# Optimization experiments

Measured on AMD Instinct MI355X. Metric: run time of the kernel, lower is better.

Reference implementation:

```python
import jax, jax.numpy as jnp
import numpy as np

HID = 64   # RNN_HID_SIZE
FEAT = 9   # feature dim, hard-coded in module
T = 36     # SEQ_LEN


def setup_inputs() -> dict:
    key = jax.random.key(0)
    ks = jax.random.split(key, 20)
    B = 16384

    def u(k, shape, stdv):
        return jax.random.uniform(k, shape, jnp.float32, -stdv, stdv)

    s_h = 1.0 / np.sqrt(HID)    # stdv for layers with 64 rows / fan-in 64
    s_f = 1.0 / np.sqrt(FEAT)   # stdv 1/3 for feature-sized layers
    s_c = 1.0 / np.sqrt(2 * FEAT)  # weight_combine: Linear(18, 9)

    inp = {
        "values": jax.random.normal(ks[0], (B, T, FEAT), jnp.float32),
        "masks": (jax.random.uniform(ks[1], (B, T, FEAT)) < 0.8).astype(jnp.float32),
        "deltas": jax.random.uniform(ks[2], (B, T, FEAT), jnp.float32, 0.0, 5.0),
        # TemporalDecay h: W [64, 9], stdv = 1/sqrt(64)
        "W_gh": u(ks[3], (HID, FEAT), s_h), "b_gh": u(ks[4], (HID,), s_h),
        # TemporalDecay x (diag): W [9, 9], stdv = 1/sqrt(9)
        "W_gx": u(ks[5], (FEAT, FEAT), s_f), "b_gx": u(ks[6], (FEAT,), s_f),
        # hist_reg: Linear(64, 9)
        "W_hist": u(ks[7], (FEAT, HID), s_h), "b_hist": u(ks[8], (FEAT,), s_h),
        "W_feat": u(ks[9], (FEAT, FEAT), s_f), "b_feat": u(ks[10], (FEAT,), s_f),
        # weight_combine: Linear(18, 9)
        "W_comb": u(ks[11], (FEAT, 2 * FEAT), s_c), "b_comb": u(ks[12], (FEAT,), s_c),
        # LSTMCell(18, 64): gates order i, f, g, o
        "W_ih": u(ks[13], (4 * HID, 2 * FEAT), s_h), "W_hh": u(ks[14], (4 * HID, HID), s_h),
        "b_ih": u(ks[15], (4 * HID,), s_h), "b_hh": u(ks[16], (4 * HID,), s_h),
    }
    return inp


def reference(values, masks, deltas, W_gh, b_gh, W_gx, b_gx, W_hist, b_hist,
              W_feat, b_feat, W_comb, b_comb, W_ih, W_hh, b_ih, b_hh):
    B = values.shape[0]
    dt = values.dtype
    eye = jnp.eye(FEAT, dtype=dt)
    Wgx_diag = W_gx * eye            # TemporalDecay diag mask
    Wfeat_off = W_feat * (1.0 - eye)

    # time-major for scan: [T, B, F]
    xs = (jnp.swapaxes(values, 0, 1), jnp.swapaxes(masks, 0, 1), jnp.swapaxes(deltas, 0, 1))

    def step(carry, xt):
        h, c, loss = carry
        x, m, d = xt
        gamma_h = jnp.exp(-jax.nn.relu(d @ W_gh.T + b_gh))   # [B, 64]
        gamma_x = jnp.exp(-jax.nn.relu(d @ Wgx_diag.T + b_gx))  # [B, 9]
        h = h * gamma_h
        x_h = h @ W_hist.T + b_hist
        denom = jnp.sum(m) + 1e-5
        x_c = m * x + (1.0 - m) * x_h
        z_h = x_c @ Wfeat_off.T + b_feat
        alpha = jnp.concatenate([gamma_x, m], axis=1) @ W_comb.T + b_comb
        c_h = alpha * z_h + (1.0 - alpha) * x_h
        loss = loss + (jnp.sum(jnp.abs(x - x_h) * m)
                       + jnp.sum(jnp.abs(x - z_h) * m)
                       + jnp.sum(jnp.abs(x - c_h) * m)) / denom
        c_c = m * x + (1.0 - m) * c_h
        inp = jnp.concatenate([c_c, m], axis=1)              # [B, 18]
        gates = inp @ W_ih.T + b_ih + h @ W_hh.T + b_hh      # [B, 256]
        i, f, g, o = jnp.split(gates, 4, axis=1)
        c = jax.nn.sigmoid(f) * c + jax.nn.sigmoid(i) * jnp.tanh(g)
        h = jax.nn.sigmoid(o) * jnp.tanh(c)
        return (h, c, loss), c_c

    init = (jnp.zeros((B, HID), dt), jnp.zeros((B, HID), dt), jnp.zeros((), dt))
    (_, _, loss), imps = jax.lax.scan(step, init, xs)
    imputations = jnp.swapaxes(imps, 0, 1)  # [B, T, F]
    return loss / T, imputations
```

## Files before the change

kernel.cpp:

```cpp
#include <hip/hip_runtime.h>

typedef _Float16 hh;
typedef _Float16 h2  __attribute__((ext_vector_type(2)));
typedef _Float16 v4h __attribute__((ext_vector_type(4)));
typedef _Float16 v8h __attribute__((ext_vector_type(8)));
typedef float v4f    __attribute__((ext_vector_type(4)));
typedef unsigned short u16;

#define T_STEPS 36
#define FEAT 9
#define HID 64
#define BT 32
#define SIN_STR 232
#define PK_STR 40

__device__ __forceinline__ float fast_exp2(float x) {
#if __has_builtin(__builtin_amdgcn_exp2f)
  return __builtin_amdgcn_exp2f(x);
#else
  return exp2f(x);
#endif
}
__device__ __forceinline__ float fast_rcp(float x) {
#if __has_builtin(__builtin_amdgcn_rcpf)
  return __builtin_amdgcn_rcpf(x);
#else
  return 1.f / x;
#endif
}
__device__ __forceinline__ float sigmoid_fast(float x) {
  return fast_rcp(1.f + fast_exp2(x * -1.442695041f));
}
__device__ __forceinline__ float tanh_fast(float x) {
  return 1.f - 2.f * fast_rcp(1.f + fast_exp2(x * 2.885390082f));
}
__device__ __forceinline__ float fdot2(h2 a, h2 b, float c) {
#if __has_builtin(__builtin_amdgcn_fdot2)
  return __builtin_amdgcn_fdot2(a, b, c, false);
#else
  return c + (float)a[0] * (float)b[0] + (float)a[1] * (float)b[1];
#endif
}
__device__ __forceinline__ h2 mkh2(hh a, hh b) { h2 r; r[0] = a; r[1] = b; return r; }
__device__ __forceinline__ v4f mfma16(v8h a, v8h b, v4f c) {
  return __builtin_amdgcn_mfma_f32_16x16x32_f16(a, b, c, 0, 0, 0);
}

__global__ void zero_ws(float* __restrict__ ws, float* __restrict__ out) {
  int tid = threadIdx.x;
  if (tid < T_STEPS) ws[tid] = 0.f;
  if (tid == 0) out[0] = 0.f;
}

__global__ __launch_bounds__(256) void denom_kernel(const float* __restrict__ masks,
                                                    float* __restrict__ ws) {
  __shared__ float red[T_STEPS];
  const int tid = threadIdx.x;
  const int e = blockIdx.x * 256 + tid;
  if (tid < T_STEPS) red[tid] = 0.f;
  float acc[T_STEPS];
#pragma unroll
  for (int t = 0; t < T_STEPS; ++t) acc[t] = 0.f;
  const float4* p = (const float4*)masks + (size_t)e * 81;
#pragma unroll
  for (int c = 0; c < 81; ++c) {
    float4 v = p[c];
    acc[(4 * c) / 9]     += v.x;
    acc[(4 * c + 1) / 9] += v.y;
    acc[(4 * c + 2) / 9] += v.z;
    acc[(4 * c + 3) / 9] += v.w;
  }
  __syncthreads();
  int rot = tid % T_STEPS;
#pragma unroll
  for (int t = 0; t < T_STEPS; ++t) {
    int tt = rot + t; if (tt >= T_STEPS) tt -= T_STEPS;
    atomicAdd(&red[tt], acc[tt]);
  }
  __syncthreads();
  if (tid < T_STEPS) atomicAdd(&ws[tid], red[tid]);
}


__global__ __launch_bounds__(256, 2) void rits_kernel(
    const float* __restrict__ values, const float* __restrict__ masks,
    const float* __restrict__ deltas,
    const float* __restrict__ W_gh, const float* __restrict__ b_gh,
    const float* __restrict__ W_gx, const float* __restrict__ b_gx,
    const float* __restrict__ W_hist, const float* __restrict__ b_hist,
    const float* __restrict__ W_feat, const float* __restrict__ b_feat,
    const float* __restrict__ W_comb, const float* __restrict__ b_comb,
    const float* __restrict__ W_ih, const float* __restrict__ W_hh,
    const float* __restrict__ b_ih, const float* __restrict__ b_hh,
    const float* __restrict__ denom, float* __restrict__ out) {

  __shared__ __align__(16) hh sIn[BT * SIN_STR];
  __shared__ __align__(16) hh sPk[BT * PK_STR];
  __shared__ float sRed[256];

  const int tid = threadIdx.x;
  const int lane = tid & 63;
  const int wid = tid >> 6;
  const int q = lane >> 4;
  const int nlo = lane & 15;
  const int b0 = blockIdx.x * BT;
  const int j_col = 16 * wid + nlo;

  v8h bG[4][3];
#pragma unroll
  for (int p = 0; p < 4; ++p)
#pragma unroll
    for (int kt = 0; kt < 3; ++kt) {
      int n = 64 * p + j_col;
      v8h r;
#pragma unroll
      for (int jj = 0; jj < 8; ++jj) {
        int k = kt * 32 + q * 8 + jj;
        float v = 0.f;
        if (k < 18)       v = W_ih[n * 18 + k];
        else if (k < 82)  v = W_hh[n * 64 + (k - 18)];
        else if (k == 82) v = b_ih[n] + b_hh[n];
        r[jj] = (hh)v;
      }
      bG[p][kt] = r;
    }
  v8h bH[3];
#pragma unroll
  for (int kt = 0; kt < 3; ++kt) {
    v8h r;
#pragma unroll
    for (int jj = 0; jj < 8; ++jj) {
      int k = kt * 32 + q * 8 + jj;
      float v = 0.f;
      if (nlo < 9) {
        if (k >= 18 && k < 82) v = W_hist[nlo * 64 + (k - 18)];
        else if (k == 82)      v = b_hist[nlo];
      }
      r[jj] = (hh)v;
    }
    bH[kt] = r;
  }
  v8h bGamA, bGamB;
  {
    int n = j_col;
    v8h ra, rb;
#pragma unroll
    for (int jj = 0; jj < 8; ++jj) {
      int k = q * 8 + jj;
      float va = 0.f, vb = 0.f;
      if (k == 2) va = b_gh[n];
      else if (k >= 16 && k < 25) va = W_gh[n * 9 + (k - 16)];
      if (k >= 2 && k < 11) vb = W_gh[n * 9 + (k - 2)];
      else if (k == 12) vb = b_gh[n];
      ra[jj] = (hh)va; rb[jj] = (hh)vb;
    }
    bGamA = ra; bGamB = rb;
  }

  const int eP = tid >> 3, fqw = tid & 7;
  h2 wf1[5], wf2[5], wc1[9], wc2[9];
  float bf1 = b_feat[fqw], bf2 = b_feat[8];
  float bc1v = b_comb[fqw], bc2v = b_comb[8];
#pragma unroll
  for (int j = 0; j < 5; ++j) {
    int i0 = 2 * j, i1 = 2 * j + 1;
    hh a0 = (hh)((i0 == fqw) ? 0.f : W_feat[fqw * 9 + i0]);
    hh a1 = (hh)((i1 < 9) ? ((i1 == fqw) ? 0.f : W_feat[fqw * 9 + i1]) : 0.f);
    wf1[j] = mkh2(a0, a1);
    hh c0 = (hh)((i0 == 8) ? 0.f : W_feat[8 * 9 + i0]);
    hh c1 = (hh)((i1 < 9) ? W_feat[8 * 9 + i1] : 0.f);
    wf2[j] = mkh2(c0, c1);
  }
#pragma unroll
  for (int j = 0; j < 9; ++j) {
    wc1[j] = mkh2((hh)W_comb[fqw * 18 + 2 * j], (hh)W_comb[fqw * 18 + 2 * j + 1]);
    wc2[j] = mkh2((hh)W_comb[8 * 18 + 2 * j], (hh)W_comb[8 * 18 + 2 * j + 1]);
  }
  float wgx[9], bgxv[9];
#pragma unroll
  for (int f = 0; f < 9; ++f) { wgx[f] = W_gx[f * 9 + f]; bgxv[f] = b_gx[f]; }

  for (int i = tid; i < BT * SIN_STR; i += 256) sIn[i] = (hh)0.f;
  __syncthreads();
  if (tid < BT) {
    sIn[tid * SIN_STR + 82] = (hh)1.f;
    sIn[tid * SIN_STR + 178] = (hh)1.f;
    sIn[tid * SIN_STR + 212] = (hh)1.f;
  }
  const int e1 = tid / 9, f1 = tid - 9 * e1;
  const int e2g = (tid + 256) / 9, f2g = (tid + 256) - 9 * e2g;
  float dreg0 = 0.f, dreg1 = 0.f;
  {
    size_t off = (size_t)(b0 + e1) * (T_STEPS * FEAT) + f1;
    sPk[e1 * PK_STR + f1] = (hh)values[off];
    sPk[e1 * PK_STR + 9 + f1] = (hh)masks[off];
    sPk[e1 * PK_STR + 27 + f1] = (hh)deltas[off];
    float d1 = deltas[off + FEAT];
    dreg0 = d1;
    sIn[e1 * SIN_STR + 202 + f1] = (hh)d1;
    if (tid < 32) {
      size_t off2 = (size_t)(b0 + e2g) * (T_STEPS * FEAT) + f2g;
      sPk[e2g * PK_STR + f2g] = (hh)values[off2];
      sPk[e2g * PK_STR + 9 + f2g] = (hh)masks[off2];
      sPk[e2g * PK_STR + 27 + f2g] = (hh)deltas[off2];
      float d1b = deltas[off2 + FEAT];
      dreg1 = d1b;
      sIn[e2g * SIN_STR + 202 + f2g] = (hh)d1b;
    }
  }
  __syncthreads();

  float c_s[8];
#pragma unroll
  for (int i = 0; i < 8; ++i) c_s[i] = 0.f;
  float loss_acc = 0.f;

  for (int t = 0; t < T_STEPS; ++t) {
    const float inv_den = fast_rcp(denom[t] + 1e-5f);

    v4f gacc[2];
    {
      const int sel = (t + 1) & 1;
      const int awin = 176 + sel * 24;
#pragma unroll
      for (int mt = 0; mt < 2; ++mt) {
        v8h a = *(const v8h*)&sIn[(mt * 16 + nlo) * SIN_STR + awin + q * 8];
        v4f z4 = {0.f, 0.f, 0.f, 0.f};
        gacc[mt] = sel ? mfma16(a, bGamB, z4) : mfma16(a, bGamA, z4);
      }
    }
    if (wid < 2) {
      const int base = (t & 1) * 96;
      v4f acc = {0.f, 0.f, 0.f, 0.f};
#pragma unroll
      for (int kt = 0; kt < 3; ++kt) {
        v8h a = *(const v8h*)&sIn[(wid * 16 + nlo) * SIN_STR + base + kt * 32 + q * 8];
        acc = mfma16(a, bH[kt], acc);
      }
      if (nlo < 9) {
#pragma unroll
        for (int r = 0; r < 4; ++r)
          sPk[(wid * 16 + q * 4 + r) * PK_STR + 18 + nlo] = (hh)acc[r];
      }
    }
    __syncthreads();

    {
      const int pk = eP * PK_STR;
      float x_f  = (float)sPk[pk + fqw];
      float m_f  = (float)sPk[pk + 9 + fqw];
      float xh_f = (float)sPk[pk + 18 + fqw];
      v8h r0 = *(const v8h*)&sPk[pk];
      v8h r1 = *(const v8h*)&sPk[pk + 8];
      v8h r2 = *(const v8h*)&sPk[pk + 16];
      v8h r3 = *(const v8h*)&sPk[pk + 24];
      v4h r4 = *(const v4h*)&sPk[pk + 32];
      hh xxh[9] = {r0[0],r0[1],r0[2],r0[3],r0[4],r0[5],r0[6],r0[7],r1[0]};
      hh mmh[9] = {r1[1],r1[2],r1[3],r1[4],r1[5],r1[6],r1[7],r2[0],r2[1]};
      hh xhh[9] = {r2[2],r2[3],r2[4],r2[5],r2[6],r2[7],r3[0],r3[1],r3[2]};
      hh ddh[9] = {r3[3],r3[4],r3[5],r3[6],r3[7],r4[0],r4[1],r4[2],r4[3]};
      hh xch[10];
#pragma unroll
      for (int f = 0; f < 9; ++f) {
        u16 mb = __builtin_bit_cast(u16, mmh[f]);
        xch[f] = mb ? xxh[f] : xhh[f];
      }
      xch[9] = (hh)0.f;
      hh gxh[9];
#pragma unroll
      for (int f = 0; f < 9; ++f) {
        float y = fmaxf((float)ddh[f] * wgx[f] + bgxv[f], 0.f);
        gxh[f] = (hh)fast_exp2(y * -1.442695041f);
      }
      h2 xc2[5] = {mkh2(xch[0],xch[1]), mkh2(xch[2],xch[3]), mkh2(xch[4],xch[5]),
                   mkh2(xch[6],xch[7]), mkh2(xch[8],xch[9])};
      h2 g2[9]  = {mkh2(gxh[0],gxh[1]), mkh2(gxh[2],gxh[3]), mkh2(gxh[4],gxh[5]),
                   mkh2(gxh[6],gxh[7]), mkh2(gxh[8],mmh[0]), mkh2(mmh[1],mmh[2]),
                   mkh2(mmh[3],mmh[4]), mkh2(mmh[5],mmh[6]), mkh2(mmh[7],mmh[8])};
      float z1 = bf1, a1 = bc1v;
#pragma unroll
      for (int j = 0; j < 5; ++j) z1 = fdot2(wf1[j], xc2[j], z1);
#pragma unroll
      for (int j = 0; j < 9; ++j) a1 = fdot2(wc1[j], g2[j], a1);
      float ch1 = xh_f + a1 * (z1 - xh_f);
      bool obs1 = (m_f != 0.f);
      float cc1 = obs1 ? x_f : ch1;
      float lterm = obs1 ? (fabsf(x_f - xh_f) + fabsf(x_f - z1) + fabsf(x_f - ch1)) : 0.f;
      const int pb = (t & 1) * 96;
      sIn[eP * SIN_STR + pb + fqw] = (hh)cc1;
      sIn[eP * SIN_STR + pb + 9 + fqw] = (hh)m_f;
      out[1 + (size_t)(b0 + eP) * (T_STEPS * FEAT) + t * FEAT + fqw] = cc1;
      if (fqw == 7) {
        float z2 = bf2, a2 = bc2v;
#pragma unroll
        for (int j = 0; j < 5; ++j) z2 = fdot2(wf2[j], xc2[j], z2);
#pragma unroll
        for (int j = 0; j < 9; ++j) a2 = fdot2(wc2[j], g2[j], a2);
        float x8 = (float)xxh[8], m8 = (float)mmh[8], xh8 = (float)xhh[8];
        float ch2 = xh8 + a2 * (z2 - xh8);
        bool obs2 = (m8 != 0.f);
        float cc2 = obs2 ? x8 : ch2;
        lterm += obs2 ? (fabsf(x8 - xh8) + fabsf(x8 - z2) + fabsf(x8 - ch2)) : 0.f;
        sIn[eP * SIN_STR + pb + 8] = (hh)cc2;
        sIn[eP * SIN_STR + pb + 17] = mmh[8];
        out[1 + (size_t)(b0 + eP) * (T_STEPS * FEAT) + t * FEAT + 8] = cc2;
      }
      loss_acc += lterm * inv_den;
    }
    __syncthreads();

    {
      float px0 = 0.f, pm0 = 0.f, px1 = 0.f, pm1 = 0.f, pd0 = 0.f, pd1 = 0.f;
      const bool pre1 = (t + 1 < T_STEPS), pre2 = (t + 2 < T_STEPS);
      if (pre1) {
        size_t off = (size_t)(b0 + e1) * (T_STEPS * FEAT) + (t + 1) * FEAT + f1;
        px0 = values[off]; pm0 = masks[off];
        if (tid < 32) {
          size_t off2 = (size_t)(b0 + e2g) * (T_STEPS * FEAT) + (t + 1) * FEAT + f2g;
          px1 = values[off2]; pm1 = masks[off2];
        }
      }
      if (pre2) {
        size_t offd = (size_t)(b0 + e1) * (T_STEPS * FEAT) + (t + 2) * FEAT + f1;
        pd0 = deltas[offd];
        if (tid < 32) {
          size_t offd2 = (size_t)(b0 + e2g) * (T_STEPS * FEAT) + (t + 2) * FEAT + f2g;
          pd1 = deltas[offd2];
        }
      }

      const int base = (t & 1) * 96;
      const int pub = ((t + 1) & 1) * 96;
      v8h af[2][3];
#pragma unroll
      for (int mt = 0; mt < 2; ++mt)
#pragma unroll
        for (int kt = 0; kt < 3; ++kt)
          af[mt][kt] = *(const v8h*)&sIn[(mt * 16 + nlo) * SIN_STR + base + kt * 32 + q * 8];

      v4f acc[2][4];
#pragma unroll
      for (int mt = 0; mt < 2; ++mt)
#pragma unroll
        for (int p = 0; p < 4; ++p)
          acc[mt][p] = (v4f){0.f, 0.f, 0.f, 0.f};
#pragma unroll
      for (int mt = 0; mt < 2; ++mt)
#pragma unroll
        for (int p = 0; p < 4; ++p)
#pragma unroll
          for (int kt = 0; kt < 3; ++kt)
            acc[mt][p] = mfma16(af[mt][kt], bG[p][kt], acc[mt][p]);

#pragma unroll
      for (int mt = 0; mt < 2; ++mt) {
#pragma unroll
        for (int r = 0; r < 4; ++r) {
          float ig = sigmoid_fast(acc[mt][0][r]);
          float fg = sigmoid_fast(acc[mt][1][r]);
          float gg = tanh_fast(acc[mt][2][r]);
          float og = sigmoid_fast(acc[mt][3][r]);
          float cn = fg * c_s[mt * 4 + r] + ig * gg;
          c_s[mt * 4 + r] = cn;
          float hn = og * tanh_fast(cn);
          float gam = fast_exp2(fmaxf(gacc[mt][r], 0.f) * -1.442695041f);
          sIn[(mt * 16 + q * 4 + r) * SIN_STR + pub + 18 + j_col] = (hh)(hn * gam);
        }
      }

      if (pre1) {
        sPk[e1 * PK_STR + f1] = (hh)px0;
        sPk[e1 * PK_STR + 9 + f1] = (hh)pm0;
        sPk[e1 * PK_STR + 27 + f1] = (hh)dreg0;
        if (tid < 32) {
          sPk[e2g * PK_STR + f2g] = (hh)px1;
          sPk[e2g * PK_STR + 9 + f2g] = (hh)pm1;
          sPk[e2g * PK_STR + 27 + f2g] = (hh)dreg1;
        }
      }
      if (pre2) {
        const int sb = 192 + (t & 1) * 10;
        sIn[e1 * SIN_STR + sb + f1] = (hh)pd0;
        dreg0 = pd0;
        if (tid < 32) { sIn[e2g * SIN_STR + sb + f2g] = (hh)pd1; dreg1 = pd1; }
      }
    }
    __syncthreads();
  }

  sRed[tid] = loss_acc;
  __syncthreads();
  for (int k = 128; k > 0; k >>= 1) {
    if (tid < k) sRed[tid] += sRed[tid + k];
    __syncthreads();
  }
  if (tid == 0) atomicAdd(out, sRed[0] * (1.f / (float)T_STEPS));
}

extern "C" void kernel_launch(void* const* d_in, const int* in_sizes, int n_in,
                              void* d_out, int out_size, void* d_ws, size_t ws_size,
                              hipStream_t stream) {
  const float* values = (const float*)d_in[0];
  const float* masks  = (const float*)d_in[1];
  const float* deltas = (const float*)d_in[2];
  const float* W_gh   = (const float*)d_in[3];
  const float* b_gh   = (const float*)d_in[4];
  const float* W_gx   = (const float*)d_in[5];
  const float* b_gx   = (const float*)d_in[6];
  const float* W_hist = (const float*)d_in[7];
  const float* b_hist = (const float*)d_in[8];
  const float* W_feat = (const float*)d_in[9];
  const float* b_feat = (const float*)d_in[10];
  const float* W_comb = (const float*)d_in[11];
  const float* b_comb = (const float*)d_in[12];
  const float* W_ih   = (const float*)d_in[13];
  const float* W_hh   = (const float*)d_in[14];
  const float* b_ih   = (const float*)d_in[15];
  const float* b_hh   = (const float*)d_in[16];

  float* out = (float*)d_out;
  float* ws  = (float*)d_ws;
  int B = in_sizes[0] / (T_STEPS * FEAT);

  zero_ws<<<1, 64, 0, stream>>>(ws, out);
  denom_kernel<<<B / 256, 256, 0, stream>>>(masks, ws);
  rits_kernel<<<B / BT, 256, 0, stream>>>(values, masks, deltas,
                                          W_gh, b_gh, W_gx, b_gx,
                                          W_hist, b_hist, W_feat, b_feat,
                                          W_comb, b_comb, W_ih, W_hh,
                                          b_ih, b_hh, ws, out);
}
```

Baseline: 292.6 us.

## Halve batch tile per block, raise occupancy, use wave shuffles for reductions

Each block of the RITS kernel now handles 16 batch rows instead of 32, so it has twice as many blocks, and the launch bound requests 4 blocks per CU. Each wave does one MFMA row tile, and the elementwise imputation stage alternates between the two wave pairs on odd and even steps. The denom kernel and the final loss reduction use wavefront shuffles in place of shared-memory atomics and tree reductions. The aim is to hide the latency of the serial 36-step recurrence through more resident blocks. The cost is half the threads sitting idle in the elementwise phase and fewer MFMAs per barrier.

```diff
diff --git a/kernel.cpp b/kernel.cpp
--- a/kernel.cpp
+++ b/kernel.cpp
@@ -10,7 +10,7 @@
 #define T_STEPS 36
 #define FEAT 9
 #define HID 64
-#define BT 32
+#define BT 16
 #define SIN_STR 232
 #define PK_STR 40
 
@@ -52,16 +52,14 @@
   if (tid == 0) out[0] = 0.f;
 }
 
-__global__ __launch_bounds__(256) void denom_kernel(const float* __restrict__ masks,
-                                                    float* __restrict__ ws) {
-  __shared__ float red[T_STEPS];
+__global__ __launch_bounds__(64) void denom_kernel(const float* __restrict__ masks,
+                                                   float* __restrict__ ws) {
   const int tid = threadIdx.x;
-  const int e = blockIdx.x * 256 + tid;
-  if (tid < T_STEPS) red[tid] = 0.f;
+  const size_t e = (size_t)blockIdx.x * 64 + tid;
+  const float4* p = (const float4*)masks + e * 81;
   float acc[T_STEPS];
 #pragma unroll
   for (int t = 0; t < T_STEPS; ++t) acc[t] = 0.f;
-  const float4* p = (const float4*)masks + (size_t)e * 81;
 #pragma unroll
   for (int c = 0; c < 81; ++c) {
     float4 v = p[c];
@@ -70,19 +68,16 @@
     acc[(4 * c + 2) / 9] += v.z;
     acc[(4 * c + 3) / 9] += v.w;
   }
-  __syncthreads();
-  int rot = tid % T_STEPS;
 #pragma unroll
   for (int t = 0; t < T_STEPS; ++t) {
-    int tt = rot + t; if (tt >= T_STEPS) tt -= T_STEPS;
-    atomicAdd(&red[tt], acc[tt]);
-  }
-  __syncthreads();
-  if (tid < T_STEPS) atomicAdd(&ws[tid], red[tid]);
-}
-
-
-__global__ __launch_bounds__(256, 2) void rits_kernel(
+    float v = acc[t];
+#pragma unroll
+    for (int s = 32; s > 0; s >>= 1) v += __shfl_down(v, s, 64);
+    if (tid == 0) atomicAdd(&ws[t], v);
+  }
+}
+
+__global__ __launch_bounds__(256, 4) void rits_kernel(
     const float* __restrict__ values, const float* __restrict__ masks,
     const float* __restrict__ deltas,
     const float* __restrict__ W_gh, const float* __restrict__ b_gh,
@@ -96,7 +91,7 @@
 
   __shared__ __align__(16) hh sIn[BT * SIN_STR];
   __shared__ __align__(16) hh sPk[BT * PK_STR];
-  __shared__ float sRed[256];
+  __shared__ float sRedW[4];
 
   const int tid = threadIdx.x;
   const int lane = tid & 63;
@@ -157,7 +152,9 @@
     bGamA = ra; bGamB = rb;
   }
 
-  const int eP = tid >> 3, fqw = tid & 7;
+  const int uP = tid & 127;
+  const int eP = uP >> 3, fqw = uP & 7;
+  const int myPair = wid >> 1;
   h2 wf1[5], wf2[5], wc1[9], wc2[9];
   float bf1 = b_feat[fqw], bf2 = b_feat[8];
   float bc1v = b_comb[fqw], bc2v = b_comb[8];
@@ -180,6 +177,9 @@
 #pragma unroll
   for (int f = 0; f < 9; ++f) { wgx[f] = W_gx[f * 9 + f]; bgxv[f] = b_gx[f]; }
 
+  float* const outp0 = out + 1 + (size_t)(b0 + eP) * (T_STEPS * FEAT) + fqw;
+  float* const outp8 = out + 1 + (size_t)(b0 + eP) * (T_STEPS * FEAT) + 8;
+
   for (int i = tid; i < BT * SIN_STR; i += 256) sIn[i] = (hh)0.f;
   __syncthreads();
   if (tid < BT) {
@@ -188,64 +188,52 @@
     sIn[tid * SIN_STR + 212] = (hh)1.f;
   }
   const int e1 = tid / 9, f1 = tid - 9 * e1;
-  const int e2g = (tid + 256) / 9, f2g = (tid + 256) - 9 * e2g;
-  float dreg0 = 0.f, dreg1 = 0.f;
-  {
+  const bool pf = (tid < BT * FEAT);
+  float dreg = 0.f;
+  if (pf) {
     size_t off = (size_t)(b0 + e1) * (T_STEPS * FEAT) + f1;
     sPk[e1 * PK_STR + f1] = (hh)values[off];
     sPk[e1 * PK_STR + 9 + f1] = (hh)masks[off];
     sPk[e1 * PK_STR + 27 + f1] = (hh)deltas[off];
     float d1 = deltas[off + FEAT];
-    dreg0 = d1;
+    dreg = d1;
     sIn[e1 * SIN_STR + 202 + f1] = (hh)d1;
-    if (tid < 32) {
-      size_t off2 = (size_t)(b0 + e2g) * (T_STEPS * FEAT) + f2g;
-      sPk[e2g * PK_STR + f2g] = (hh)values[off2];
-      sPk[e2g * PK_STR + 9 + f2g] = (hh)masks[off2];
-      sPk[e2g * PK_STR + 27 + f2g] = (hh)deltas[off2];
-      float d1b = deltas[off2 + FEAT];
-      dreg1 = d1b;
-      sIn[e2g * SIN_STR + 202 + f2g] = (hh)d1b;
-    }
   }
   __syncthreads();
 
-  float c_s[8];
-#pragma unroll
-  for (int i = 0; i < 8; ++i) c_s[i] = 0.f;
+  float c_s[4];
+#pragma unroll
+  for (int i = 0; i < 4; ++i) c_s[i] = 0.f;
   float loss_acc = 0.f;
 
   for (int t = 0; t < T_STEPS; ++t) {
     const float inv_den = fast_rcp(denom[t] + 1e-5f);
 
-    v4f gacc[2];
+    v4f gacc;
     {
       const int sel = (t + 1) & 1;
       const int awin = 176 + sel * 24;
-#pragma unroll
-      for (int mt = 0; mt < 2; ++mt) {
-        v8h a = *(const v8h*)&sIn[(mt * 16 + nlo) * SIN_STR + awin + q * 8];
-        v4f z4 = {0.f, 0.f, 0.f, 0.f};
-        gacc[mt] = sel ? mfma16(a, bGamB, z4) : mfma16(a, bGamA, z4);
-      }
-    }
-    if (wid < 2) {
+      v8h a = *(const v8h*)&sIn[nlo * SIN_STR + awin + q * 8];
+      v4f z4 = {0.f, 0.f, 0.f, 0.f};
+      gacc = sel ? mfma16(a, bGamB, z4) : mfma16(a, bGamA, z4);
+    }
+    if (wid == 0) {
       const int base = (t & 1) * 96;
       v4f acc = {0.f, 0.f, 0.f, 0.f};
 #pragma unroll
       for (int kt = 0; kt < 3; ++kt) {
-        v8h a = *(const v8h*)&sIn[(wid * 16 + nlo) * SIN_STR + base + kt * 32 + q * 8];
+        v8h a = *(const v8h*)&sIn[nlo * SIN_STR + base + kt * 32 + q * 8];
         acc = mfma16(a, bH[kt], acc);
       }
       if (nlo < 9) {
 #pragma unroll
         for (int r = 0; r < 4; ++r)
-          sPk[(wid * 16 + q * 4 + r) * PK_STR + 18 + nlo] = (hh)acc[r];
+          sPk[(q * 4 + r) * PK_STR + 18 + nlo] = (hh)acc[r];
       }
     }
     __syncthreads();
 
-    {
+    if (myPair == (t & 1)) {
       const int pk = eP * PK_STR;
       float x_f  = (float)sPk[pk + fqw];
       float m_f  = (float)sPk[pk + 9 + fqw];
@@ -289,7 +277,7 @@
       const int pb = (t & 1) * 96;
       sIn[eP * SIN_STR + pb + fqw] = (hh)cc1;
       sIn[eP * SIN_STR + pb + 9 + fqw] = (hh)m_f;
-      out[1 + (size_t)(b0 + eP) * (T_STEPS * FEAT) + t * FEAT + fqw] = cc1;
+      outp0[t * FEAT] = cc1;
       if (fqw == 7) {
         float z2 = bf2, a2 = bc2v;
 #pragma unroll
@@ -303,98 +291,77 @@
         lterm += obs2 ? (fabsf(x8 - xh8) + fabsf(x8 - z2) + fabsf(x8 - ch2)) : 0.f;
         sIn[eP * SIN_STR + pb + 8] = (hh)cc2;
         sIn[eP * SIN_STR + pb + 17] = mmh[8];
-        out[1 + (size_t)(b0 + eP) * (T_STEPS * FEAT) + t * FEAT + 8] = cc2;
+        outp8[t * FEAT] = cc2;
       }
       loss_acc += lterm * inv_den;
     }
     __syncthreads();
 
     {
-      float px0 = 0.f, pm0 = 0.f, px1 = 0.f, pm1 = 0.f, pd0 = 0.f, pd1 = 0.f;
-      const bool pre1 = (t + 1 < T_STEPS), pre2 = (t + 2 < T_STEPS);
+      float px = 0.f, pm = 0.f, pd = 0.f;
+      const bool pre1 = pf && (t + 1 < T_STEPS);
+      const bool pre2 = pf && (t + 2 < T_STEPS);
       if (pre1) {
         size_t off = (size_t)(b0 + e1) * (T_STEPS * FEAT) + (t + 1) * FEAT + f1;
-        px0 = values[off]; pm0 = masks[off];
-        if (tid < 32) {
-          size_t off2 = (size_t)(b0 + e2g) * (T_STEPS * FEAT) + (t + 1) * FEAT + f2g;
-          px1 = values[off2]; pm1 = masks[off2];
-        }
+        px = values[off]; pm = masks[off];
       }
       if (pre2) {
         size_t offd = (size_t)(b0 + e1) * (T_STEPS * FEAT) + (t + 2) * FEAT + f1;
-        pd0 = deltas[offd];
-        if (tid < 32) {
-          size_t offd2 = (size_t)(b0 + e2g) * (T_STEPS * FEAT) + (t + 2) * FEAT + f2g;
-          pd1 = deltas[offd2];
-        }
+        pd = deltas[offd];
       }
 
       const int base = (t & 1) * 96;
       const int pub = ((t + 1) & 1) * 96;
-      v8h af[2][3];
-#pragma unroll
-      for (int mt = 0; mt < 2; ++mt)
+      v8h af[3];
+#pragma unroll
+      for (int kt = 0; kt < 3; ++kt)
+        af[kt] = *(const v8h*)&sIn[nlo * SIN_STR + base + kt * 32 + q * 8];
+
+      v4f acc[4];
+#pragma unroll
+      for (int p = 0; p < 4; ++p) acc[p] = (v4f){0.f, 0.f, 0.f, 0.f};
+#pragma unroll
+      for (int p = 0; p < 4; ++p)
 #pragma unroll
         for (int kt = 0; kt < 3; ++kt)
-          af[mt][kt] = *(const v8h*)&sIn[(mt * 16 + nlo) * SIN_STR + base + kt * 32 + q * 8];
-
-      v4f acc[2][4];
-#pragma unroll
-      for (int mt = 0; mt < 2; ++mt)
-#pragma unroll
-        for (int p = 0; p < 4; ++p)
-          acc[mt][p] = (v4f){0.f, 0.f, 0.f, 0.f};
-#pragma unroll
-      for (int mt = 0; mt < 2; ++mt)
-#pragma unroll
-        for (int p = 0; p < 4; ++p)
-#pragma unroll
-          for (int kt = 0; kt < 3; ++kt)
-            acc[mt][p] = mfma16(af[mt][kt], bG[p][kt], acc[mt][p]);
-
-#pragma unroll
-      for (int mt = 0; mt < 2; ++mt) {
-#pragma unroll
-        for (int r = 0; r < 4; ++r) {
-          float ig = sigmoid_fast(acc[mt][0][r]);
-          float fg = sigmoid_fast(acc[mt][1][r]);
-          float gg = tanh_fast(acc[mt][2][r]);
-          float og = sigmoid_fast(acc[mt][3][r]);
-          float cn = fg * c_s[mt * 4 + r] + ig * gg;
-          c_s[mt * 4 + r] = cn;
-          float hn = og * tanh_fast(cn);
-          float gam = fast_exp2(fmaxf(gacc[mt][r], 0.f) * -1.442695041f);
-          sIn[(mt * 16 + q * 4 + r) * SIN_STR + pub + 18 + j_col] = (hh)(hn * gam);
-        }
+          acc[p] = mfma16(af[kt], bG[p][kt], acc[p]);
+
+#pragma unroll
+      for (int r = 0; r < 4; ++r) {
+        float ig = sigmoid_fast(acc[0][r]);
+        float fg = sigmoid_fast(acc[1][r]);
+        float gg = tanh_fast(acc[2][r]);
+        float og = sigmoid_fast(acc[3][r]);
+        float cn = fg * c_s[r] + ig * gg;
+        c_s[r] = cn;
+        float hn = og * tanh_fast(cn);
+        float gam = fast_exp2(fmaxf(gacc[r], 0.f) * -1.442695041f);
+        sIn[(q * 4 + r) * SIN_STR + pub + 18 + j_col] = (hh)(hn * gam);
       }
 
       if (pre1) {
-        sPk[e1 * PK_STR + f1] = (hh)px0;
-        sPk[e1 * PK_STR + 9 + f1] = (hh)pm0;
-        sPk[e1 * PK_STR + 27 + f1] = (hh)dreg0;
-        if (tid < 32) {
-          sPk[e2g * PK_STR + f2g] = (hh)px1;
-          sPk[e2g * PK_STR + 9 + f2g] = (hh)pm1;
-          sPk[e2g * PK_STR + 27 + f2g] = (hh)dreg1;
-        }
+        sPk[e1 * PK_STR + f1] = (hh)px;
+        sPk[e1 * PK_STR + 9 + f1] = (hh)pm;
+        sPk[e1 * PK_STR + 27 + f1] = (hh)dreg;
       }
       if (pre2) {
         const int sb = 192 + (t & 1) * 10;
-        sIn[e1 * SIN_STR + sb + f1] = (hh)pd0;
-        dreg0 = pd0;
-        if (tid < 32) { sIn[e2g * SIN_STR + sb + f2g] = (hh)pd1; dreg1 = pd1; }
+        sIn[e1 * SIN_STR + sb + f1] = (hh)pd;
+        dreg = pd;
       }
     }
     __syncthreads();
   }
 
-  sRed[tid] = loss_acc;
-  __syncthreads();
-  for (int k = 128; k > 0; k >>= 1) {
-    if (tid < k) sRed[tid] += sRed[tid + k];
+  {
+    float v = loss_acc;
+#pragma unroll
+    for (int s = 32; s > 0; s >>= 1) v += __shfl_down(v, s, 64);
+    if (lane == 0) sRedW[wid] = v;
     __syncthreads();
-  }
-  if (tid == 0) atomicAdd(out, sRed[0] * (1.f / (float)T_STEPS));
+    if (tid == 0)
+      atomicAdd(out, (sRedW[0] + sRedW[1] + sRedW[2] + sRedW[3]) * (1.f / (float)T_STEPS));
+  }
 }
 
 extern "C" void kernel_launch(void* const* d_in, const int* in_sizes, int n_in,
@@ -423,7 +390,7 @@
   int B = in_sizes[0] / (T_STEPS * FEAT);
 
   zero_ws<<<1, 64, 0, stream>>>(ws, out);
-  denom_kernel<<<B / 256, 256, 0, stream>>>(masks, ws);
+  denom_kernel<<<B / 64, 64, 0, stream>>>(masks, ws);
   rits_kernel<<<B / BT, 256, 0, stream>>>(values, masks, deltas,
                                           W_gh, b_gh, W_gx, b_gx,
                                           W_hist, b_hist, W_feat, b_feat,
```

Result: slower. 622.6 us (+112.8%).
